# Kernel optimization log

Measured on AMD Instinct MI355X. Metric: run time of the kernel, lower is better.

The kernel has to match this reference:

```python
import jax, jax.numpy as jnp
import numpy as np

THETA = 10000.0
AXES_DIM = (16, 56, 56)  # sums to head_dim=128
HEADS = 24
HEAD_DIM = 128
EPS = 1e-5


def _pos_embed(ids):
    # ids: (S, n_axes) int -> cos, sin each (S, head_dim//2)
    pos = ids.astype(jnp.float32)
    cos_out, sin_out = [], []
    for i, d in enumerate(AXES_DIM):
        freqs = 1.0 / (THETA ** (jnp.arange(0, d, 2, dtype=jnp.float32) / d))  # (d/2,)
        ang = pos[:, i][:, None] * freqs[None, :]  # (S, d/2)
        cos_out.append(jnp.cos(ang))
        sin_out.append(jnp.sin(ang))
    return jnp.concatenate(cos_out, -1), jnp.concatenate(sin_out, -1)


def _rms_norm(x, w):
    # per-head RMSNorm over last dim (head_dim)
    var = jnp.mean(x * x, axis=-1, keepdims=True)
    return x * jax.lax.rsqrt(var + EPS) * w


def _apply_rope(x, cos, sin):
    # non-neox (interleaved) rotary. x: (B,S,H,D), cos/sin: (S,D/2)
    x1 = x[..., 0::2]
    x2 = x[..., 1::2]
    c = cos[None, :, None, :]
    s = sin[None, :, None, :]
    o1 = x1 * c - x2 * s
    o2 = x2 * c + x1 * s
    return jnp.stack([o1, o2], axis=-1).reshape(x.shape)


def setup_inputs() -> dict:
    key = jax.random.key(0)
    ks = jax.random.split(key, 12)
    B, S_img, S_txt, D = 1, 2048, 512, 3072
    sd = 1.0 / np.sqrt(D)
    return {
        "hidden_states": jax.random.normal(ks[0], (B, S_img, D), jnp.float32),
        "encoder_hidden_states": jax.random.normal(ks[1], (B, S_txt, D), jnp.float32),
        "ids": jax.random.randint(ks[2], (S_txt + S_img, 3), 0, 64, jnp.int32),
        "w_qkv": jax.random.normal(ks[3], (D, 3 * D), jnp.float32) * sd,
        "w_add_qkv": jax.random.normal(ks[4], (D, 3 * D), jnp.float32) * sd,
        "b_add_qkv": jax.random.normal(ks[5], (3 * D,), jnp.float32) * 0.02,
        "w_out": jax.random.normal(ks[6], (D, D), jnp.float32) * sd,
        "b_out": jax.random.normal(ks[7], (D,), jnp.float32) * 0.02,
        "w_add_out": jax.random.normal(ks[8], (D, D), jnp.float32) * sd,
        "b_add_out": jax.random.normal(ks[9], (D,), jnp.float32) * 0.02,
        "norm_q_w": jnp.ones((HEAD_DIM,), jnp.float32),
        "norm_k_w": jnp.ones((HEAD_DIM,), jnp.float32),
        "norm_add_q_w": jnp.ones((HEAD_DIM,), jnp.float32),
        "norm_add_k_w": jnp.ones((HEAD_DIM,), jnp.float32),
    }


def reference(hidden_states, encoder_hidden_states, ids, w_qkv, w_add_qkv,
              b_add_qkv, w_out, b_out, w_add_out, b_add_out,
              norm_q_w, norm_k_w, norm_add_q_w, norm_add_k_w):
    B, S_img, D = hidden_states.shape
    S_txt = encoder_hidden_states.shape[1]
    H, Dh = HEADS, HEAD_DIM

    # fused QKV projections
    qkv = hidden_states @ w_qkv  # (B, S_img, 3D)
    q, k, v = jnp.split(qkv, 3, axis=-1)
    q = _rms_norm(q.reshape(B, S_img, H, Dh), norm_q_w)
    k = _rms_norm(k.reshape(B, S_img, H, Dh), norm_k_w)
    v = v.reshape(B, S_img, H, Dh)

    eqkv = encoder_hidden_states @ w_add_qkv + b_add_qkv
    eq, ek, ev = jnp.split(eqkv, 3, axis=-1)
    eq = _rms_norm(eq.reshape(B, S_txt, H, Dh), norm_add_q_w)
    ek = _rms_norm(ek.reshape(B, S_txt, H, Dh), norm_add_k_w)
    ev = ev.reshape(B, S_txt, H, Dh)

    # joint sequence: text first, then image
    q = jnp.concatenate([eq, q], axis=1)
    k = jnp.concatenate([ek, k], axis=1)
    v = jnp.concatenate([ev, v], axis=1)

    # multi-axis RoPE over joint positions
    cos, sin = _pos_embed(ids)  # (S_txt+S_img, Dh/2)
    q = _apply_rope(q, cos, sin)
    k = _apply_rope(k, cos, sin)

    # scaled dot-product attention (non-causal)
    scale = 1.0 / np.sqrt(Dh)
    scores = jnp.einsum("bqhd,bkhd->bhqk", q, k) * scale
    probs = jax.nn.softmax(scores, axis=-1)
    attn = jnp.einsum("bhqk,bkhd->bqhd", probs, v)
    attn = attn.reshape(B, S_txt + S_img, H * Dh)

    enc_out = attn[:, :S_txt] @ w_add_out + b_add_out
    img_out = attn[:, S_txt:] @ w_out + b_out
    return img_out, enc_out
```

## Files before the change

### kernel.cpp

```cpp
#include <hip/hip_runtime.h>

typedef __attribute__((ext_vector_type(8))) short short8;
typedef __attribute__((ext_vector_type(4))) short short4v;
typedef __attribute__((ext_vector_type(4))) float floatx4;

__device__ __forceinline__ float b2f(short b) {
  union { unsigned u; float f; } v; v.u = ((unsigned)(unsigned short)b) << 16; return v.f;
}
__device__ __forceinline__ short f2b(float f) {
  union { float f; unsigned u; } v; v.f = f;
  return (short)((v.u + 0x7fffu + ((v.u >> 16) & 1u)) >> 16);
}
__device__ __forceinline__ unsigned cvtpk(float lo, float hi) {
  unsigned r;
  asm("v_cvt_pk_bf16_f32 %0, %1, %2" : "=v"(r) : "v"(lo), "v"(hi));
  return r;
}
__device__ __forceinline__ float loadf(const void* p, size_t i, bool f32) {
  return f32 ? ((const float*)p)[i] : b2f(((const short*)p)[i]);
}
__device__ __forceinline__ short8 load8(const void* p, size_t i, bool f32) {
  if (f32) {
    const float* fp = (const float*)p + i;
    float4 a = *(const float4*)fp;
    float4 b = *(const float4*)(fp + 4);
    short8 r;
    r[0] = f2b(a.x); r[1] = f2b(a.y); r[2] = f2b(a.z); r[3] = f2b(a.w);
    r[4] = f2b(b.x); r[5] = f2b(b.y); r[6] = f2b(b.z); r[7] = f2b(b.w);
    return r;
  }
  return *(const short8*)((const short*)p + i);
}

__device__ __forceinline__ void gload16(const short* g, short* l) {
  __builtin_amdgcn_global_load_lds(
      (const __attribute__((address_space(1))) unsigned int*)g,
      (__attribute__((address_space(3))) unsigned int*)l, 16, 0, 0);
}

__global__ void detect_dtype(const unsigned short* __restrict__ w, int* __restrict__ flag) {
  __shared__ int cnt;
  if (threadIdx.x == 0) cnt = 0;
  __syncthreads();
  int bad = 0;
  for (int i = threadIdx.x; i < 4096; i += 256) {
    int e = (w[i] >> 7) & 0xFF;
    if (e >= 0xC8) bad++;
  }
  atomicAdd(&cnt, bad);
  __syncthreads();
  if (threadIdx.x == 0) *flag = (cnt > 64) ? 1 : 0;
}

__global__ __launch_bounds__(256)
void cvt_bf16(const void* __restrict__ src, short* __restrict__ dst, long n8,
              const int* __restrict__ dflag) {
  const bool f32 = (*dflag != 0);
  long stride = (long)gridDim.x * 256;
  for (long i = (long)blockIdx.x * 256 + threadIdx.x; i < n8; i += stride) {
    long e = i * 8;
    if (f32) {
      const float* fp = (const float*)src + e;
      float4 a = *(const float4*)fp;
      float4 b = *(const float4*)(fp + 4);
      short8 r;
      r[0] = f2b(a.x); r[1] = f2b(a.y); r[2] = f2b(a.z); r[3] = f2b(a.w);
      r[4] = f2b(b.x); r[5] = f2b(b.y); r[6] = f2b(b.z); r[7] = f2b(b.w);
      *(short8*)(dst + e) = r;
    } else {
      *(short8*)(dst + e) = *(const short8*)((const short*)src + e);
    }
  }
}

__global__ __launch_bounds__(256)
void cvt_t(const void* __restrict__ src, short* __restrict__ dst,
           int K, int N, const int* __restrict__ dflag) {
  __shared__ short st[64][72];
  const bool f32 = (*dflag != 0);
  const int n0 = blockIdx.x << 6, k0 = blockIdx.y << 6;
  const int c4 = threadIdx.x & 15;
  const int rq = threadIdx.x >> 4;
#pragma unroll
  for (int r = 0; r < 4; ++r) {
    int k = r * 16 + rq;
    int n = c4 * 4;
    short v0, v1, v2, v3;
    if (f32) {
      const float* sp = (const float*)src + (size_t)(k0 + k) * N + n0 + n;
      float4 f = *(const float4*)sp;
      v0 = f2b(f.x); v1 = f2b(f.y); v2 = f2b(f.z); v3 = f2b(f.w);
    } else {
      const short* sp = (const short*)src + (size_t)(k0 + k) * N + n0 + n;
      short4v s = *(const short4v*)sp;
      v0 = s[0]; v1 = s[1]; v2 = s[2]; v3 = s[3];
    }
    st[n + 0][k] = v0; st[n + 1][k] = v1; st[n + 2][k] = v2; st[n + 3][k] = v3;
  }
  __syncthreads();
  const int n = threadIdx.x >> 2;
  const int kc = (threadIdx.x & 3) << 4;
  short8 a = *(const short8*)(&st[n][kc]);
  short8 b = *(const short8*)(&st[n][kc + 8]);
  short* dp = dst + (size_t)(n0 + n) * K + k0 + kc;
  *(short8*)(dp) = a;
  *(short8*)(dp + 8) = b;
}

__global__ __launch_bounds__(256, 2)
void gemm_bt(const void* __restrict__ A, int a_row0,
             const void* __restrict__ B, const void* __restrict__ bias,
             void* __restrict__ C, int c_row0, int N, int K,
             const int* __restrict__ dflag, int aIn, int cOut) {
  __shared__ short As[128 * 32];
  __shared__ short Bs[128 * 32];
  const bool f32 = (*dflag != 0);
  const bool a32 = aIn && f32;
  const bool c32 = cOut && f32;
  const int tid = threadIdx.x;
  const int lane = tid & 63, w = tid >> 6;
  const int wm = w & 1, wn = w >> 1;
  const int qg = lane >> 4, l16 = lane & 15;
  const int m0 = blockIdx.y << 7, n0 = blockIdx.x << 7;

  const int arow = tid >> 2, ak = (tid & 3) << 3;
  const int brow = tid >> 4, bc = (tid & 15) << 3;
  const int rot = tid & 15;

  floatx4 acc[4][4];
#pragma unroll
  for (int i = 0; i < 4; ++i)
#pragma unroll
    for (int j = 0; j < 4; ++j) acc[i][j] = (floatx4){0.f, 0.f, 0.f, 0.f};

  for (int k0 = 0; k0 < K; k0 += 32) {
    __syncthreads();
#pragma unroll
    for (int j = 0; j < 2; ++j) {
      short8 av = load8(A, (size_t)(a_row0 + m0 + j * 64 + arow) * K + (k0 + ak), a32);
      *(short8*)(As + (j * 64 + arow) * 32 + ak) = av;
      int kr = j * 16 + brow;
      short8 bv = load8(B, (size_t)(k0 + kr) * N + (n0 + bc), f32);
      int kq = kr >> 3, kj = kr & 7;
#pragma unroll
      for (int s = 0; s < 8; ++s) {
        int u = (s + rot) & 7;
        int n = bc + u;
        Bs[(n << 5) + ((kq ^ (n & 3)) << 3) + kj] = bv[u];
      }
    }
    __syncthreads();
    short8 a[4];
#pragma unroll
    for (int mi = 0; mi < 4; ++mi)
      a[mi] = *(const short8*)(As + (wm * 64 + mi * 16 + l16) * 32 + qg * 8);
#pragma unroll
    for (int ni = 0; ni < 4; ++ni) {
      int n = wn * 64 + ni * 16 + l16;
      short8 b = *(const short8*)(Bs + (n << 5) + ((qg ^ (n & 3)) << 3));
#pragma unroll
      for (int mi = 0; mi < 4; ++mi)
        acc[mi][ni] = __builtin_amdgcn_mfma_f32_16x16x32_bf16(a[mi], b, acc[mi][ni], 0, 0, 0);
    }
  }
#pragma unroll
  for (int ni = 0; ni < 4; ++ni) {
    int col = n0 + wn * 64 + ni * 16 + l16;
    float bv = bias ? loadf(bias, col, f32) : 0.0f;
#pragma unroll
    for (int mi = 0; mi < 4; ++mi) {
      int row = m0 + wm * 64 + mi * 16 + qg * 4;
#pragma unroll
      for (int r = 0; r < 4; ++r) {
        size_t idx = (size_t)(c_row0 + row + r) * N + col;
        float val = acc[mi][ni][r] + bv;
        if (c32) ((float*)C)[idx] = val;
        else     ((short*)C)[idx] = f2b(val);
      }
    }
  }
}

__global__ __launch_bounds__(256, 3)
void gemm_bf2(const short* __restrict__ A,
              const short* __restrict__ BTa, const void* __restrict__ biasa,
              int a0a, int c0a, int nYa,
              const short* __restrict__ BTb, const void* __restrict__ biasb,
              int a0b, int c0b,
              void* __restrict__ C, int N, int K,
              const int* __restrict__ dflag, int cOut) {
  __shared__ short As[3][128 * 32];
  __shared__ short Bs[3][128 * 32];
  const bool f32 = (*dflag != 0);
  const bool c32 = cOut && f32;
  const int y = blockIdx.y;
  const short* BT; const void* bias; int arow0, crow0;
  if (y < nYa) { BT = BTa; bias = biasa; arow0 = a0a + (y << 7); crow0 = c0a + (y << 7); }
  else { int my = y - nYa; BT = BTb; bias = biasb; arow0 = a0b + (my << 7); crow0 = c0b + (my << 7); }
  const int tid = threadIdx.x;
  const int lane = tid & 63, w = tid >> 6;
  const int wm = w & 1, wn = w >> 1;
  const int qg = lane >> 4, l16 = lane & 15;
  const int n0 = blockIdx.x << 7;
  const int garow = lane >> 2;
  const int gcir = lane & 3;
  const int nk = K >> 5;
  const int swz = (gcir ^ (garow & 3) ^ (garow >> 2)) << 3;
  const short* Abase = A + (size_t)(arow0 + w * 32 + garow) * K + swz;
  const short* Bbase = BT + (size_t)(n0 + w * 32 + garow) * K + swz;
  const int rswz = (l16 & 3) ^ (l16 >> 2);

  floatx4 acc[4][4];
#pragma unroll
  for (int i = 0; i < 4; ++i)
#pragma unroll
    for (int j = 0; j < 4; ++j) acc[i][j] = (floatx4){0.f, 0.f, 0.f, 0.f};

  auto STAGE = [&](int buf, int k0) {
#pragma unroll
    for (int j = 0; j < 2; ++j) {
      gload16(Abase + (size_t)j * 16 * K + k0, &As[buf][(w * 2 + j) << 9]);
      gload16(Bbase + (size_t)j * 16 * K + k0, &Bs[buf][(w * 2 + j) << 9]);
    }
  };

  STAGE(0, 0);
  if (nk > 1) STAGE(1, 32);

  int cb = 0;
  for (int t = 0; t < nk; ++t) {
    if (t + 2 < nk) {
      int sb = (cb == 0) ? 2 : cb - 1;
      STAGE(sb, (t + 2) << 5);
      asm volatile("s_waitcnt vmcnt(8)" ::: "memory");
    } else if (t + 1 < nk) {
      asm volatile("s_waitcnt vmcnt(4)" ::: "memory");
    } else {
      asm volatile("s_waitcnt vmcnt(0)" ::: "memory");
    }
    __builtin_amdgcn_s_barrier();
    short8 a[4], b[4];
#pragma unroll
    for (int mi = 0; mi < 4; ++mi) {
      int ra = wm * 64 + mi * 16 + l16;
      a[mi] = *(const short8*)(&As[cb][(ra << 5) + ((qg ^ rswz) << 3)]);
    }
#pragma unroll
    for (int ni = 0; ni < 4; ++ni) {
      int n = wn * 64 + ni * 16 + l16;
      b[ni] = *(const short8*)(&Bs[cb][(n << 5) + ((qg ^ rswz) << 3)]);
    }
    __builtin_amdgcn_s_setprio(1);
#pragma unroll
    for (int ni = 0; ni < 4; ++ni)
#pragma unroll
      for (int mi = 0; mi < 4; ++mi)
        acc[mi][ni] = __builtin_amdgcn_mfma_f32_16x16x32_bf16(a[mi], b[ni], acc[mi][ni], 0, 0, 0);
    __builtin_amdgcn_s_setprio(0);
    asm volatile("s_waitcnt lgkmcnt(0)" ::: "memory");
    __builtin_amdgcn_s_barrier();
    cb = (cb == 2) ? 0 : cb + 1;
  }
#pragma unroll
  for (int ni = 0; ni < 4; ++ni) {
    int col = n0 + wn * 64 + ni * 16 + l16;
    float bvv = bias ? loadf(bias, col, f32) : 0.0f;
#pragma unroll
    for (int mi = 0; mi < 4; ++mi) {
      int row = wm * 64 + mi * 16 + qg * 4;
#pragma unroll
      for (int r = 0; r < 4; ++r) {
        size_t idx = (size_t)(crow0 + row + r) * N + col;
        float val = acc[mi][ni][r] + bvv;
        if (c32) ((float*)C)[idx] = val;
        else     ((short*)C)[idx] = f2b(val);
      }
    }
  }
}

__global__ __launch_bounds__(512)
void norm_rope(short* __restrict__ qkv, const int* __restrict__ ids,
               const void* __restrict__ nqw, const void* __restrict__ nkw,
               const void* __restrict__ naqw, const void* __restrict__ nakw,
               const int* __restrict__ dflag) {
  const bool f32 = (*dflag != 0);
  const int t = blockIdx.x, wv = threadIdx.x >> 6, lane = threadIdx.x & 63;
  const bool txt = t < 512;
  int p = lane, axis; float expo;
  if (p < 8)       { axis = 0; expo = (float)(2 * p) * (1.0f / 16.0f); }
  else if (p < 36) { axis = 1; expo = (float)(2 * (p - 8)) * (1.0f / 56.0f); }
  else             { axis = 2; expo = (float)(2 * (p - 36)) * (1.0f / 56.0f); }
  float freq = __expf(-expo * 9.210340371976184f);
  float ang = (float)ids[t * 3 + axis] * freq;
  float s, c; sincosf(ang, &s, &c);
  const void* qw = txt ? naqw : nqw;
  const void* kw = txt ? nakw : nkw;
  float w0q = loadf(qw, 2 * lane, f32), w1q = loadf(qw, 2 * lane + 1, f32);
  float w0k = loadf(kw, 2 * lane, f32), w1k = loadf(kw, 2 * lane + 1, f32);
  const float QS = 0.08838834764831845f * 1.4426950408889634f;
#pragma unroll
  for (int i = 0; i < 3; ++i) {
    int h = wv + 8 * i;
    short* qp = qkv + (size_t)t * 9216 + h * 128 + 2 * lane;
    short* kp = qp + 3072;
    union { unsigned u; short sh[2]; } qv, kv;
    qv.u = *(const unsigned*)qp;
    kv.u = *(const unsigned*)kp;
    float q0 = b2f(qv.sh[0]), q1 = b2f(qv.sh[1]);
    float k0 = b2f(kv.sh[0]), k1 = b2f(kv.sh[1]);
    float sq = q0 * q0 + q1 * q1, sk = k0 * k0 + k1 * k1;
#pragma unroll
    for (int o = 1; o < 64; o <<= 1) { sq += __shfl_xor(sq, o); sk += __shfl_xor(sk, o); }
    float rq = rsqrtf(sq * (1.0f / 128.0f) + 1e-5f);
    float rk = rsqrtf(sk * (1.0f / 128.0f) + 1e-5f);
    float qn0 = q0 * rq * w0q, qn1 = q1 * rq * w1q;
    float kn0 = k0 * rk * w0k, kn1 = k1 * rk * w1k;
    float qo0 = qn0 * c - qn1 * s, qo1 = qn1 * c + qn0 * s;
    float ko0 = kn0 * c - kn1 * s, ko1 = kn1 * c + kn0 * s;
    union { unsigned u; short sh[2]; } qo, ko;
    qo.sh[0] = f2b(qo0 * QS);
    qo.sh[1] = f2b(qo1 * QS);
    ko.sh[0] = f2b(ko0); ko.sh[1] = f2b(ko1);
    *(unsigned*)qp = qo.u;
    *(unsigned*)kp = ko.u;
  }
}

__global__ __launch_bounds__(512, 2)
void attn_fa(const short* __restrict__ qkv, short* __restrict__ attn) {
  __shared__ short QPs[256 * 128];
  __shared__ short KVs[2][128 * 128];
  const int wgid = blockIdx.x;
  const int xcd = wgid & 7, slot = wgid >> 3;
  const int h = xcd * 3 + slot / 10;
  const int qt = slot % 10;
  const int tid = threadIdx.x, lane = tid & 63, w = tid >> 6;
  const int qg = lane >> 4, l16 = lane & 15;
  const int lr = lane >> 4, lc = lane & 15;
  const int q0 = qt << 8;
  const int sc = tid & 15;
  const int srow5 = (tid >> 4) & 15, half = tid >> 8;

  const short* Qg  = qkv + (size_t)q0 * 9216 + h * 128;
  const short* Kg0 = qkv + 3072 + h * 128;
  const short* Vg0 = qkv + 6144 + h * 128;

  short8 vr[4];
#pragma unroll
  for (int j = 0; j < 8; ++j) {
    int row = j * 32 + w * 4 + lr;
    gload16(Qg + (size_t)row * 9216 + ((lc ^ (row & 7)) << 3),
            QPs + (j * 32 + w * 4) * 128);
  }
#pragma unroll
  for (int j = 0; j < 4; ++j) {
    int row = j * 32 + w * 4 + lr;
    gload16(Kg0 + (size_t)row * 9216 + ((lc ^ (row & 7)) << 3),
            &KVs[0][(j * 32 + w * 4) * 128]);
  }
#pragma unroll
  for (int j = 0; j < 4; ++j) {
    int row = half * 64 + j * 16 + srow5;
    vr[j] = *(const short8*)(Vg0 + (size_t)row * 9216 + sc * 8);
  }
  asm volatile("s_waitcnt vmcnt(8) lgkmcnt(0)" ::: "memory");
  __builtin_amdgcn_s_barrier();
  short8 aq[2][4];
#pragma unroll
  for (int mi = 0; mi < 2; ++mi)
#pragma unroll
    for (int kc = 0; kc < 4; ++kc) {
      int row = w * 32 + mi * 16 + l16;
      aq[mi][kc] = *(const short8*)(QPs + row * 128 + (((kc * 4 + qg) ^ (row & 7)) << 3));
    }

  floatx4 acc_o[2][8];
#pragma unroll
  for (int mi = 0; mi < 2; ++mi)
#pragma unroll
    for (int nd = 0; nd < 8; ++nd) acc_o[mi][nd] = (floatx4){0.f, 0.f, 0.f, 0.f};
  float m_i[2][4], l_i[2][4];
#pragma unroll
  for (int mi = 0; mi < 2; ++mi)
#pragma unroll
    for (int r = 0; r < 4; ++r) { m_i[mi][r] = -1e30f; l_i[mi][r] = 0.0f; }

  for (int kt = 0; kt < 20; ++kt) {
    const int c = kt & 1;
    asm volatile("s_waitcnt vmcnt(4) lgkmcnt(0)" ::: "memory");
    __builtin_amdgcn_s_barrier();
    if (kt < 19) {
      const short* Kg = qkv + ((size_t)(kt + 1) * 128) * 9216 + 3072 + h * 128;
#pragma unroll
      for (int j = 0; j < 4; ++j) {
        int row = j * 32 + w * 4 + lr;
        gload16(Kg + (size_t)row * 9216 + ((lc ^ (row & 7)) << 3),
                &KVs[1 - c][(j * 32 + w * 4) * 128]);
      }
    }
    floatx4 acc_s[2][8];
#pragma unroll
    for (int mi = 0; mi < 2; ++mi)
#pragma unroll
      for (int ni = 0; ni < 8; ++ni) acc_s[mi][ni] = (floatx4){0.f, 0.f, 0.f, 0.f};
    __builtin_amdgcn_s_setprio(1);
#pragma unroll
    for (int kc = 0; kc < 4; ++kc) {
#pragma unroll
      for (int ni = 0; ni < 8; ++ni) {
        int row = ni * 16 + l16;
        short8 b = *(const short8*)(&KVs[c][row * 128 + (((kc * 4 + qg) ^ (row & 7)) << 3)]);
        acc_s[0][ni] = __builtin_amdgcn_mfma_f32_16x16x32_bf16(aq[0][kc], b, acc_s[0][ni], 0, 0, 0);
        acc_s[1][ni] = __builtin_amdgcn_mfma_f32_16x16x32_bf16(aq[1][kc], b, acc_s[1][ni], 0, 0, 0);
      }
    }
    __builtin_amdgcn_s_setprio(0);
    float alpha[2][4];
#pragma unroll
    for (int mi = 0; mi < 2; ++mi) {
#pragma unroll
      for (int r = 0; r < 4; ++r) {
        float mx = acc_s[mi][0][r];
#pragma unroll
        for (int ni = 1; ni < 8; ++ni) mx = fmaxf(mx, acc_s[mi][ni][r]);
        mx = fmaxf(mx, __shfl_xor(mx, 1));
        mx = fmaxf(mx, __shfl_xor(mx, 2));
        mx = fmaxf(mx, __shfl_xor(mx, 4));
        mx = fmaxf(mx, __shfl_xor(mx, 8));
        float mn = fmaxf(m_i[mi][r], mx);
        alpha[mi][r] = __builtin_amdgcn_exp2f(m_i[mi][r] - mn);
        m_i[mi][r] = mn;
      }
    }
#pragma unroll
    for (int mi = 0; mi < 2; ++mi) {
      float rs[4] = {0.f, 0.f, 0.f, 0.f};
#pragma unroll
      for (int r = 0; r < 4; ++r) {
        float pv[8];
#pragma unroll
        for (int ni = 0; ni < 8; ++ni) {
          pv[ni] = __builtin_amdgcn_exp2f(acc_s[mi][ni][r] - m_i[mi][r]);
          rs[r] += pv[ni];
        }
        unsigned u0 = cvtpk(pv[0], pv[1]);
        unsigned u1 = cvtpk(pv[2], pv[3]);
        unsigned u2 = cvtpk(pv[4], pv[5]);
        unsigned u3 = cvtpk(pv[6], pv[7]);
        int row = w * 32 + mi * 16 + qg * 4 + r;
        uint4 uu; uu.x = u0; uu.y = u1; uu.z = u2; uu.w = u3;
        *(uint4*)(QPs + row * 128 + ((l16 ^ (row & 15)) << 3)) = uu;
      }
#pragma unroll
      for (int r = 0; r < 4; ++r) {
        float t = rs[r];
        t += __shfl_xor(t, 1); t += __shfl_xor(t, 2);
        t += __shfl_xor(t, 4); t += __shfl_xor(t, 8);
        l_i[mi][r] = alpha[mi][r] * l_i[mi][r] + t;
      }
#pragma unroll
      for (int nd = 0; nd < 8; ++nd)
#pragma unroll
        for (int r = 0; r < 4; ++r) acc_o[mi][nd][r] *= alpha[mi][r];
    }
    asm volatile("s_waitcnt lgkmcnt(0)" ::: "memory");
    __builtin_amdgcn_s_barrier();
#pragma unroll
    for (int u = 0; u < 8; ++u) {
      int d = sc * 8 + u;
      short4v pk = { vr[0][u], vr[1][u], vr[2][u], vr[3][u] };
      *(short4v*)(&KVs[c][d * 128 + (((srow5 ^ u ^ (sc & 7))) << 3) + half * 4]) = pk;
    }
    if (kt < 19) {
      const short* Vg = qkv + ((size_t)(kt + 1) * 128) * 9216 + 6144 + h * 128;
#pragma unroll
      for (int j = 0; j < 4; ++j) {
        int row = half * 64 + j * 16 + srow5;
        vr[j] = *(const short8*)(Vg + (size_t)row * 9216 + sc * 8);
      }
    }
    asm volatile("s_waitcnt lgkmcnt(0)" ::: "memory");
    __builtin_amdgcn_s_barrier();
    __builtin_amdgcn_s_setprio(1);
#pragma unroll
    for (int kc = 0; kc < 4; ++kc) {
      int prow0 = w * 32 + l16;
      short8 ap0 = *(const short8*)(QPs + prow0 * 128 + (((kc * 4 + qg) ^ (prow0 & 15)) << 3));
      int prow1 = prow0 + 16;
      short8 ap1 = *(const short8*)(QPs + prow1 * 128 + (((kc * 4 + qg) ^ (prow1 & 15)) << 3));
#pragma unroll
      for (int nd = 0; nd < 8; ++nd) {
        int row = nd * 16 + l16;
        int chn = (kc * 4 + qg) ^ (row & 7) ^ ((row >> 3) & 7);
        short8 b = *(const short8*)(&KVs[c][row * 128 + (chn << 3)]);
        acc_o[0][nd] = __builtin_amdgcn_mfma_f32_16x16x32_bf16(ap0, b, acc_o[0][nd], 0, 0, 0);
        acc_o[1][nd] = __builtin_amdgcn_mfma_f32_16x16x32_bf16(ap1, b, acc_o[1][nd], 0, 0, 0);
      }
    }
    __builtin_amdgcn_s_setprio(0);
  }
#pragma unroll
  for (int mi = 0; mi < 2; ++mi) {
    float inv[4];
#pragma unroll
    for (int r = 0; r < 4; ++r) inv[r] = 1.0f / l_i[mi][r];
#pragma unroll
    for (int nd = 0; nd < 8; ++nd) {
#pragma unroll
      for (int r = 0; r < 4; ++r) {
        int row = w * 32 + mi * 16 + qg * 4 + r;
        QPs[row * 128 + nd * 16 + l16] = f2b(acc_o[mi][nd][r] * inv[r]);
      }
    }
  }
  asm volatile("s_waitcnt lgkmcnt(0)" ::: "memory");
#pragma unroll
  for (int j = 0; j < 8; ++j) {
    int rrow = w * 32 + j * 4 + qg;
    short8 vv = *(const short8*)(QPs + rrow * 128 + l16 * 8);
    *(short8*)(attn + (size_t)(q0 + rrow) * 3072 + h * 128 + l16 * 8) = vv;
  }
}

extern "C" void kernel_launch(void* const* d_in, const int* in_sizes, int n_in,
                              void* d_out, int out_size, void* d_ws, size_t ws_size,
                              hipStream_t stream) {
  (void)in_sizes; (void)n_in; (void)out_size;
  const void* hidden    = d_in[0];
  const void* enc       = d_in[1];
  const int*  ids       = (const int*)d_in[2];
  const void* w_qkv     = d_in[3];
  const void* w_add_qkv = d_in[4];
  const void* b_add_qkv = d_in[5];
  const void* w_out     = d_in[6];
  const void* b_out     = d_in[7];
  const void* w_add_out = d_in[8];
  const void* b_add_out = d_in[9];
  const void* nqw  = d_in[10];
  const void* nkw  = d_in[11];
  const void* naqw = d_in[12];
  const void* nakw = d_in[13];

  int*   dflag = (int*)d_ws;
  short* qkv   = (short*)((char*)d_ws + 256);
  short* attnB = qkv + (size_t)2560 * 9216;

  short* pool  = attnB + (size_t)2560 * 3072;
  const long n_hid  = 2048L * 3072;
  const long n_enc  = 512L * 3072;
  const long n_wqkv = 3072L * 9216;
  const long n_wout = 3072L * 3072;
  short* xb   = pool;
  short* wqb  = xb + n_enc + n_hid;
  short* waqb = wqb + n_wqkv;
  short* wob  = waqb + n_wqkv;
  short* waob = wob + n_wout;
  const size_t REQ = 256 + 2 * ((size_t)2560 * 9216 + (size_t)2560 * 3072 +
                                n_hid + n_enc + 2 * n_wqkv + 2 * n_wout);

  detect_dtype<<<1, 256, 0, stream>>>((const unsigned short*)w_qkv, dflag);

  if (ws_size >= REQ) {
    cvt_bf16<<<256, 256, 0, stream>>>(enc, xb, n_enc / 8, dflag);
    cvt_bf16<<<1024, 256, 0, stream>>>(hidden, xb + n_enc, n_hid / 8, dflag);
    cvt_t<<<dim3(144, 48), 256, 0, stream>>>(w_qkv,     wqb,  3072, 9216, dflag);
    cvt_t<<<dim3(144, 48), 256, 0, stream>>>(w_add_qkv, waqb, 3072, 9216, dflag);
    cvt_t<<<dim3(48, 48), 256, 0, stream>>>(w_out,     wob,  3072, 3072, dflag);
    cvt_t<<<dim3(48, 48), 256, 0, stream>>>(w_add_out, waob, 3072, 3072, dflag);

    gemm_bf2<<<dim3(72, 20), 256, 0, stream>>>(
        xb, waqb, b_add_qkv, 0, 0, 4, wqb, nullptr, 512, 512,
        qkv, 9216, 3072, dflag, 0);
    norm_rope<<<dim3(2560), 512, 0, stream>>>(qkv, ids, nqw, nkw, naqw, nakw, dflag);
    attn_fa<<<dim3(240), 512, 0, stream>>>(qkv, attnB);
    gemm_bf2<<<dim3(24, 20), 256, 0, stream>>>(
        attnB, wob, b_out, 512, 0, 16, waob, b_add_out, 0, 2048,
        d_out, 3072, 3072, dflag, 1);
  } else {
    gemm_bt<<<dim3(72, 4), 256, 0, stream>>>(enc, 0, w_add_qkv, b_add_qkv, qkv, 0, 9216, 3072, dflag, 1, 0);
    gemm_bt<<<dim3(72, 16), 256, 0, stream>>>(hidden, 0, w_qkv, nullptr, qkv, 512, 9216, 3072, dflag, 1, 0);
    norm_rope<<<dim3(2560), 512, 0, stream>>>(qkv, ids, nqw, nkw, naqw, nakw, dflag);
    attn_fa<<<dim3(240), 512, 0, stream>>>(qkv, attnB);
    gemm_bt<<<dim3(24, 16), 256, 0, stream>>>(attnB, 512, w_out, b_out, d_out, 0, 3072, 3072, dflag, 0, 1);
    gemm_bt<<<dim3(24, 4), 256, 0, stream>>>(attnB, 0, w_add_out, b_add_out, d_out, 2048, 3072, 3072, dflag, 0, 1);
  }
}
```

Baseline: 842.4 us.

## Merge conversion launches, single-barrier GEMM pipeline, lazy softmax rescale

Folds the six conversion launches into three by batching paired inputs through a grid z-dimension or a combined index range, which cuts launch overhead. The GEMM main loop now uses one barrier per k-step and issues the next stage's loads after that barrier instead of keeping two barriers. The flash-attention loop skips the running-max rescale of the output accumulator and row sum unless some row's new max exceeds the old one by more than 8 in log2 units, saving exp and multiply work. The lazy rescale lets unnormalized exponentials grow up to 2^8 before correction, which adds bf16 and fp32 range and precision risk.

```diff
diff --git a/kernel.cpp b/kernel.cpp
--- a/kernel.cpp
+++ b/kernel.cpp
@@ -53,31 +53,37 @@
 }
 
 __global__ __launch_bounds__(256)
-void cvt_bf16(const void* __restrict__ src, short* __restrict__ dst, long n8,
-              const int* __restrict__ dflag) {
+void cvt_bf16_2(const void* __restrict__ srcA, long n8A,
+                const void* __restrict__ srcB, long n8B,
+                short* __restrict__ dst, const int* __restrict__ dflag) {
   const bool f32 = (*dflag != 0);
+  const long n8 = n8A + n8B;
   long stride = (long)gridDim.x * 256;
   for (long i = (long)blockIdx.x * 256 + threadIdx.x; i < n8; i += stride) {
-    long e = i * 8;
+    const void* s; long e;
+    if (i < n8A) { s = srcA; e = i * 8; } else { s = srcB; e = (i - n8A) * 8; }
     if (f32) {
-      const float* fp = (const float*)src + e;
+      const float* fp = (const float*)s + e;
       float4 a = *(const float4*)fp;
       float4 b = *(const float4*)(fp + 4);
       short8 r;
       r[0] = f2b(a.x); r[1] = f2b(a.y); r[2] = f2b(a.z); r[3] = f2b(a.w);
       r[4] = f2b(b.x); r[5] = f2b(b.y); r[6] = f2b(b.z); r[7] = f2b(b.w);
-      *(short8*)(dst + e) = r;
+      *(short8*)(dst + i * 8) = r;
     } else {
-      *(short8*)(dst + e) = *(const short8*)((const short*)src + e);
+      *(short8*)(dst + i * 8) = *(const short8*)((const short*)s + e);
     }
   }
 }
 
 __global__ __launch_bounds__(256)
-void cvt_t(const void* __restrict__ src, short* __restrict__ dst,
-           int K, int N, const int* __restrict__ dflag) {
+void cvt_t2(const void* __restrict__ src0, short* __restrict__ dst0,
+            const void* __restrict__ src1, short* __restrict__ dst1,
+            int K, int N, const int* __restrict__ dflag) {
   __shared__ short st[64][72];
   const bool f32 = (*dflag != 0);
+  const void* src = blockIdx.z ? src1 : src0;
+  short* dst = blockIdx.z ? dst1 : dst0;
   const int n0 = blockIdx.x << 6, k0 = blockIdx.y << 6;
   const int c4 = threadIdx.x & 15;
   const int rq = threadIdx.x >> 4;
@@ -229,16 +235,16 @@
 
   int cb = 0;
   for (int t = 0; t < nk; ++t) {
+    if (t + 1 < nk) {
+      asm volatile("s_waitcnt vmcnt(4) lgkmcnt(0)" ::: "memory");
+    } else {
+      asm volatile("s_waitcnt vmcnt(0) lgkmcnt(0)" ::: "memory");
+    }
+    __builtin_amdgcn_s_barrier();
     if (t + 2 < nk) {
       int sb = (cb == 0) ? 2 : cb - 1;
       STAGE(sb, (t + 2) << 5);
-      asm volatile("s_waitcnt vmcnt(8)" ::: "memory");
-    } else if (t + 1 < nk) {
-      asm volatile("s_waitcnt vmcnt(4)" ::: "memory");
-    } else {
-      asm volatile("s_waitcnt vmcnt(0)" ::: "memory");
-    }
-    __builtin_amdgcn_s_barrier();
+    }
     short8 a[4], b[4];
 #pragma unroll
     for (int mi = 0; mi < 4; ++mi) {
@@ -257,8 +263,6 @@
       for (int mi = 0; mi < 4; ++mi)
         acc[mi][ni] = __builtin_amdgcn_mfma_f32_16x16x32_bf16(a[mi], b[ni], acc[mi][ni], 0, 0, 0);
     __builtin_amdgcn_s_setprio(0);
-    asm volatile("s_waitcnt lgkmcnt(0)" ::: "memory");
-    __builtin_amdgcn_s_barrier();
     cb = (cb == 2) ? 0 : cb + 1;
   }
 #pragma unroll
@@ -416,7 +420,8 @@
       }
     }
     __builtin_amdgcn_s_setprio(0);
-    float alpha[2][4];
+    float mxv[2][4];
+    bool need = false;
 #pragma unroll
     for (int mi = 0; mi < 2; ++mi) {
 #pragma unroll
@@ -428,9 +433,22 @@
         mx = fmaxf(mx, __shfl_xor(mx, 2));
         mx = fmaxf(mx, __shfl_xor(mx, 4));
         mx = fmaxf(mx, __shfl_xor(mx, 8));
-        float mn = fmaxf(m_i[mi][r], mx);
-        alpha[mi][r] = __builtin_amdgcn_exp2f(m_i[mi][r] - mn);
-        m_i[mi][r] = mn;
+        mxv[mi][r] = mx;
+        need = need || (mx > m_i[mi][r] + 8.0f);
+      }
+    }
+    if (__ballot(need)) {
+#pragma unroll
+      for (int mi = 0; mi < 2; ++mi) {
+#pragma unroll
+        for (int r = 0; r < 4; ++r) {
+          float mn = fmaxf(m_i[mi][r], mxv[mi][r]);
+          float al = __builtin_amdgcn_exp2f(m_i[mi][r] - mn);
+          m_i[mi][r] = mn;
+          l_i[mi][r] *= al;
+#pragma unroll
+          for (int nd = 0; nd < 8; ++nd) acc_o[mi][nd][r] *= al;
+        }
       }
     }
 #pragma unroll
@@ -457,12 +475,8 @@
         float t = rs[r];
         t += __shfl_xor(t, 1); t += __shfl_xor(t, 2);
         t += __shfl_xor(t, 4); t += __shfl_xor(t, 8);
-        l_i[mi][r] = alpha[mi][r] * l_i[mi][r] + t;
-      }
-#pragma unroll
-      for (int nd = 0; nd < 8; ++nd)
-#pragma unroll
-        for (int r = 0; r < 4; ++r) acc_o[mi][nd][r] *= alpha[mi][r];
+        l_i[mi][r] += t;
+      }
     }
     asm volatile("s_waitcnt lgkmcnt(0)" ::: "memory");
     __builtin_amdgcn_s_barrier();
@@ -562,12 +576,9 @@
   detect_dtype<<<1, 256, 0, stream>>>((const unsigned short*)w_qkv, dflag);
 
   if (ws_size >= REQ) {
-    cvt_bf16<<<256, 256, 0, stream>>>(enc, xb, n_enc / 8, dflag);
-    cvt_bf16<<<1024, 256, 0, stream>>>(hidden, xb + n_enc, n_hid / 8, dflag);
-    cvt_t<<<dim3(144, 48), 256, 0, stream>>>(w_qkv,     wqb,  3072, 9216, dflag);
-    cvt_t<<<dim3(144, 48), 256, 0, stream>>>(w_add_qkv, waqb, 3072, 9216, dflag);
-    cvt_t<<<dim3(48, 48), 256, 0, stream>>>(w_out,     wob,  3072, 3072, dflag);
-    cvt_t<<<dim3(48, 48), 256, 0, stream>>>(w_add_out, waob, 3072, 3072, dflag);
+    cvt_bf16_2<<<1024, 256, 0, stream>>>(enc, n_enc / 8, hidden, n_hid / 8, xb, dflag);
+    cvt_t2<<<dim3(144, 48, 2), 256, 0, stream>>>(w_qkv, wqb, w_add_qkv, waqb, 3072, 9216, dflag);
+    cvt_t2<<<dim3(48, 48, 2), 256, 0, stream>>>(w_out, wob, w_add_out, waob, 3072, 3072, dflag);
 
     gemm_bf2<<<dim3(72, 20), 256, 0, stream>>>(
         xb, waqb, b_add_qkv, 0, 0, 4, wqb, nullptr, 512, 512,
```

Measured after the change: 840.6 us. About the same (-0.2%).
